# Kernel optimization log

Hardware: AMD Instinct MI355X
Metric: run time of the kernel (lower is better)

The kernel has to match this reference:

```python
import jax, jax.numpy as jnp
import numpy as np

B, S, E = 512, 200, 128
H, D = 4, 32  # att_head_nums, singlehead_emb_size; H*D == E (required by residual)
FF = 4 * H * D


def setup_inputs() -> dict:
    key = jax.random.key(0)
    ks = jax.random.split(key, 12)
    sc = 0.02
    return {
        "queries": jax.random.normal(ks[0], (B, S, E), jnp.float32),
        "keys": jax.random.normal(ks[1], (B, S, E), jnp.float32),
        "keys_mask": jax.random.randint(ks[2], (B, S), 0, 2) > 0,
        "Wq": jax.random.normal(ks[3], (H * D, E), jnp.float32) * sc,
        "bq": jnp.zeros((H * D,), jnp.float32),
        "Wk": jax.random.normal(ks[4], (H * D, E), jnp.float32) * sc,
        "bk": jnp.zeros((H * D,), jnp.float32),
        "Wv": jax.random.normal(ks[5], (H * D, E), jnp.float32) * sc,
        "bv": jnp.zeros((H * D,), jnp.float32),
        "W1": jax.random.normal(ks[6], (FF, H * D), jnp.float32) * sc,
        "b1": jnp.zeros((FF,), jnp.float32),
        "W2": jax.random.normal(ks[7], (H * D, FF), jnp.float32) * sc,
        "b2": jnp.zeros((H * D,), jnp.float32),
    }


def reference(queries, keys, keys_mask, Wq, bq, Wk, bk, Wv, bv, W1, b1, W2, b2):
    # QKV projections (nn.Linear: x @ W.T + b)
    Q = queries @ Wq.T + bq                         # [B,S,H*D]
    K = keys @ Wk.T + bk
    V = keys @ Wv.T + bv
    Qh = Q.reshape(B, S, H, D).transpose(0, 2, 1, 3)  # [B,H,S,D]
    Kh = K.reshape(B, S, H, D).transpose(0, 2, 1, 3)
    Vh = V.reshape(B, S, H, D).transpose(0, 2, 1, 3)
    scores = jnp.einsum('bhqd,bhkd->bhqk', Qh, Kh) / jnp.sqrt(jnp.float32(D))
    scores = jnp.where(keys_mask[:, None, None, :], scores, -jnp.inf)
    probs = jax.nn.softmax(scores, axis=-1)
    out = jnp.einsum('bhqk,bhkd->bhqd', probs, Vh)   # [B,H,S,D]
    out = out.transpose(0, 2, 1, 3).reshape(B, S, H * D)
    out = out + queries                              # residual (use_res=True)
    # FFN with residual (use_feed_forward=True, no layer norm, dropout=0)
    ff = jax.nn.relu(out @ W1.T + b1) @ W2.T + b2
    return ff + out
```

## Files before the change

kernel.cpp:

```cpp
#include <hip/hip_runtime.h>

#define B_  512
#define S_  200
#define M_  102400

typedef short bf16x8 __attribute__((ext_vector_type(8)));
typedef float f32x4  __attribute__((ext_vector_type(4)));
typedef unsigned short u16;
typedef u16 us4 __attribute__((ext_vector_type(4)));
typedef unsigned int u32;

#define MFMA16 __builtin_amdgcn_mfma_f32_16x16x32_bf16
#define GLDS(gp, lp) __builtin_amdgcn_global_load_lds( \
    (const __attribute__((address_space(1))) unsigned int*)(gp), \
    (__attribute__((address_space(3))) unsigned int*)(lp), 16, 0, 0)

__device__ __forceinline__ u16 f2bf(float f) {
    union { float f; unsigned u; } v; v.f = f;
    unsigned r = v.u + 0x7fffu + ((v.u >> 16) & 1u);
    return (u16)(r >> 16);
}
__device__ __forceinline__ float bf2f(u16 x) {
    union { unsigned u; float f; } v; v.u = ((unsigned)x) << 16;
    return v.f;
}
__device__ __forceinline__ u32 pk(float a, float b) {
    return (__float_as_uint(a) >> 16) | (__float_as_uint(b) & 0xffff0000u);
}
__device__ __forceinline__ int swz(int row, int b) { return b ^ ((row & 7) << 4); }

#define WQ_OFF   0
#define WK_OFF   16384
#define WV_OFF   32768
#define W1_OFF   49152
#define W2_OFF   114688
#define BQS_OFF  180224
#define QB_OFF   262144
#define KB_OFF   (QB_OFF + 13107200)
#define VB_OFF   (KB_OFF + 13107200)

__global__ __launch_bounds__(256) void cvt_kernel(
    const float* __restrict__ Wq, const float* __restrict__ bq,
    const float* __restrict__ Wk, const float* __restrict__ Wv,
    const float* __restrict__ W1, const float* __restrict__ W2,
    u16* __restrict__ wdst, float* __restrict__ bqs)
{
    const float QSC = 0.17677669529663689f * 1.4426950408889634f;
    int idx = blockIdx.x * 256 + threadIdx.x;
    if (idx < 128) bqs[idx] = bq[idx] * QSC;
    if (idx < 49152) {
        int wsel = idx >> 14, r = (idx >> 7) & 127, c = idx & 127;
        const float* src = wsel == 0 ? Wq : (wsel == 1 ? Wk : Wv);
        float v = src[idx & 16383];
        if (wsel == 0) v *= QSC;
        *(u16*)((char*)(wdst + wsel * 16384) + r * 256 + swz(r, 2 * c)) = f2bf(v);
    } else if (idx < 114688) {
        int i = idx - 49152;
        int r_g = i >> 7, c = i & 127;
        int sub = r_g >> 6, fr = r_g & 63;
        *(u16*)((char*)(wdst + W1_OFF) + sub * 16384 + fr * 256 + ((2 * c) ^ ((fr & 7) << 4)))
            = f2bf(W1[i]);
    } else if (idx < 180224) {
        int i = idx - 114688;
        int r_out = i >> 9, c_ff = i & 511;
        int sub = c_ff >> 6, o = c_ff & 63;
        int chunk = o >> 5, w32 = o & 31;
        int bb = w32 >> 4, hh = (w32 >> 2) & 3, rr = w32 & 3;
        int lc = chunk * 32 + 8 * hh + 4 * bb + rr;
        *(u16*)((char*)(wdst + W2_OFF) + sub * 16384 + r_out * 128 + ((2 * lc) ^ ((r_out & 7) << 4)))
            = f2bf(W2[i]);
    }
}

__global__ __launch_bounds__(256) void proj_q_kernel(
    const float* __restrict__ X, const u16* __restrict__ Ws,
    const float* __restrict__ bqs, u16* __restrict__ Y)
{
    __shared__ __align__(16) u16 sW[16384];
    const int tid = threadIdx.x, w = tid >> 6, lane = tid & 63;
    const int lo = lane & 15, hi = lane >> 4;
    const int base = blockIdx.x * 128;

#pragma unroll
    for (int k = 0; k < 8; ++k) {
        int seg = w * 8 + k;
        GLDS((const char*)Ws + seg * 1024 + lane * 16, (char*)sW + seg * 1024);
    }

    bf16x8 a[2][4];
#pragma unroll
    for (int t = 0; t < 2; ++t) {
        const float* rp = X + (size_t)(base + w * 32 + t * 16 + lo) * 128;
#pragma unroll
        for (int ks = 0; ks < 4; ++ks) {
            float4 v0 = *(const float4*)(rp + ks * 32 + hi * 8);
            float4 v1 = *(const float4*)(rp + ks * 32 + hi * 8 + 4);
            union { bf16x8 v; u16 s[8]; } af;
            af.s[0]=f2bf(v0.x); af.s[1]=f2bf(v0.y); af.s[2]=f2bf(v0.z); af.s[3]=f2bf(v0.w);
            af.s[4]=f2bf(v1.x); af.s[5]=f2bf(v1.y); af.s[6]=f2bf(v1.z); af.s[7]=f2bf(v1.w);
            a[t][ks] = af.v;
        }
    }
    asm volatile("s_waitcnt vmcnt(0)" ::: "memory");
    __builtin_amdgcn_s_barrier();

#pragma unroll
    for (int n = 0; n < 8; ++n) {
        bf16x8 bf[4];
#pragma unroll
        for (int ks = 0; ks < 4; ++ks)
            bf[ks] = *(const bf16x8*)((const char*)sW + (n*16+lo)*256 + swz(lo, ks*64 + hi*16));
        float bb = bqs[n * 16 + lo];
#pragma unroll
        for (int t = 0; t < 2; ++t) {
            f32x4 acc = {0.f, 0.f, 0.f, 0.f};
#pragma unroll
            for (int ks = 0; ks < 4; ++ks) acc = MFMA16(a[t][ks], bf[ks], acc, 0, 0, 0);
#pragma unroll
            for (int r = 0; r < 4; ++r) {
                int row = base + w * 32 + t * 16 + hi * 4 + r;
                *(u16*)((char*)Y + (size_t)row * 256 + swz(row, n * 32 + 2 * lo)) =
                    f2bf(acc[r] + bb);
            }
        }
    }
}

__global__ __launch_bounds__(256) void proj_kv_kernel(
    const float* __restrict__ X, const u16* __restrict__ Wks, const u16* __restrict__ Wvs,
    const float* __restrict__ bk, const float* __restrict__ bv,
    u16* __restrict__ K, u16* __restrict__ V)
{
    __shared__ __align__(16) u16 sWk[16384];
    __shared__ __align__(16) u16 sWv[16384];
    const int tid = threadIdx.x, w = tid >> 6, lane = tid & 63;
    const int lo = lane & 15, hi = lane >> 4;
    const int base = blockIdx.x * 128;

#pragma unroll
    for (int k = 0; k < 8; ++k) {
        int seg = w * 8 + k;
        GLDS((const char*)Wks + seg * 1024 + lane * 16, (char*)sWk + seg * 1024);
        GLDS((const char*)Wvs + seg * 1024 + lane * 16, (char*)sWv + seg * 1024);
    }

    bf16x8 a[2][4];
#pragma unroll
    for (int t = 0; t < 2; ++t) {
        const float* rp = X + (size_t)(base + w * 32 + t * 16 + lo) * 128;
#pragma unroll
        for (int ks = 0; ks < 4; ++ks) {
            float4 v0 = *(const float4*)(rp + ks * 32 + hi * 8);
            float4 v1 = *(const float4*)(rp + ks * 32 + hi * 8 + 4);
            union { bf16x8 v; u16 s[8]; } af;
            af.s[0]=f2bf(v0.x); af.s[1]=f2bf(v0.y); af.s[2]=f2bf(v0.z); af.s[3]=f2bf(v0.w);
            af.s[4]=f2bf(v1.x); af.s[5]=f2bf(v1.y); af.s[6]=f2bf(v1.z); af.s[7]=f2bf(v1.w);
            a[t][ks] = af.v;
        }
    }
    asm volatile("s_waitcnt vmcnt(0)" ::: "memory");
    __builtin_amdgcn_s_barrier();

#pragma unroll
    for (int n = 0; n < 8; ++n) {
        bf16x8 bf[4];
#pragma unroll
        for (int ks = 0; ks < 4; ++ks)
            bf[ks] = *(const bf16x8*)((const char*)sWk + (n*16+lo)*256 + swz(lo, ks*64 + hi*16));
        float bb = bk[n * 16 + lo];
#pragma unroll
        for (int t = 0; t < 2; ++t) {
            f32x4 acc = {0.f, 0.f, 0.f, 0.f};
#pragma unroll
            for (int ks = 0; ks < 4; ++ks) acc = MFMA16(a[t][ks], bf[ks], acc, 0, 0, 0);
#pragma unroll
            for (int r = 0; r < 4; ++r) {
                size_t row = base + w * 32 + t * 16 + hi * 4 + r;
                K[row * 128 + n * 16 + lo] = f2bf(acc[r] + bb);
            }
        }
    }
#pragma unroll
    for (int n = 0; n < 8; ++n) {
        bf16x8 bf[4];
#pragma unroll
        for (int ks = 0; ks < 4; ++ks)
            bf[ks] = *(const bf16x8*)((const char*)sWv + (n*16+lo)*256 + swz(lo, ks*64 + hi*16));
        float bb = bv[n * 16 + lo];
#pragma unroll
        for (int t = 0; t < 2; ++t) {
            f32x4 acc = {0.f, 0.f, 0.f, 0.f};
#pragma unroll
            for (int ks = 0; ks < 4; ++ks) acc = MFMA16(a[t][ks], bf[ks], acc, 0, 0, 0);
#pragma unroll
            for (int r = 0; r < 4; ++r) {
                size_t row = base + w * 32 + t * 16 + hi * 4 + r;
                V[row * 128 + n * 16 + lo] = f2bf(acc[r] + bb);
            }
        }
    }
}

__global__ __launch_bounds__(256, 4) void attn_kernel(
    const u16* __restrict__ Qb, const u16* __restrict__ Kb, const u16* __restrict__ Vb,
    const int* __restrict__ mask, const float* __restrict__ queries, u16* __restrict__ Xb)
{
    __shared__ __align__(16) u16 sK[224][40];
    __shared__ __align__(16) u16 sVt[32][248];
    __shared__ __align__(16) u16 sMk[224];
    __shared__ u16 sIdx[224];
    __shared__ int sCnt4[4];

    const int bid = blockIdx.x;
    const int wg  = (bid & 7) * 256 + (bid >> 3);
    const int b   = wg >> 2;
    const int h   = wg & 3;
    const int tid = threadIdx.x;
    const int w = tid >> 6, lane = tid & 63;
    const int lo = lane & 15, hi = lane >> 4;
    const size_t rowbase = (size_t)b * 200;

    bool valid = (tid < 200) && (mask[rowbase + tid] != 0);
    unsigned long long bal = __ballot(valid);
    int prefix = __popcll(bal & ((1ull << lane) - 1ull));
    if (lane == 0) sCnt4[w] = __popcll(bal);
    __syncthreads();

    int c0_ = sCnt4[0], c1_ = sCnt4[1], c2_ = sCnt4[2], c3_ = sCnt4[3];
    int off = (w > 0 ? c0_ : 0) + (w > 1 ? c1_ : 0) + (w > 2 ? c2_ : 0);
    const int cnt = c0_ + c1_ + c2_ + c3_;
    const int cntPad = (cnt + 31) & ~31;
    const int nch = cntPad >> 5;
    if (valid) sIdx[off + prefix] = (u16)tid;
    for (int i = tid; i < 224; i += 256) {
        int cb = i & ~31, local = i & 31;
        int hh = local >> 3, j = local & 7;
        int slot = cb + 16 * (j >> 2) + 4 * hh + (j & 3);
        sMk[i] = (slot < cnt) ? (u16)0x3F80 : (u16)0;
    }
    __syncthreads();

    for (int i = tid; i < (cntPad << 2); i += 256) {
        int j = i >> 2, part = i & 3;
        bf16x8 val = {0,0,0,0,0,0,0,0};
        if (j < cnt) {
            int key = sIdx[j];
            val = *(const bf16x8*)(Kb + (rowbase + key) * 128 + h * 32 + part * 8);
        }
        *(bf16x8*)&sK[j][part * 8] = val;
    }
    for (int slot = tid; slot < (cntPad << 3); slot += 256) {
        int d = slot & 31, sg = slot >> 5;
        int s0 = sg * 4;
        int cb = s0 & ~31, a = (s0 & 31) >> 2;
        int pos = cb + (a & 3) * 8 + (a >> 2) * 4;
        us4 v;
#pragma unroll
        for (int j = 0; j < 4; ++j) {
            int s = s0 + j;
            v[j] = (s < cnt) ? Vb[(rowbase + sIdx[s]) * 128 + h * 32 + d] : (u16)0;
        }
        *(us4*)&sVt[d][pos] = v;
    }
    __syncthreads();

    for (int qb = w; qb < 13; qb += 4) {
        int qrow = qb * 16 + lo;
        if (qrow > 199) qrow = 199;
        bf16x8 qf = *(const bf16x8*)((const char*)Qb + (size_t)(rowbase + qrow) * 256
                                      + swz(qrow, h * 64 + hi * 16));

        f32x4 acc0 = {0.f, 0.f, 0.f, 0.f};
        f32x4 acc1 = {0.f, 0.f, 0.f, 0.f};
        f32x4 accs = {0.f, 0.f, 0.f, 0.f};

#pragma unroll 1
        for (int kt = 0; kt < nch; ++kt) {
            int cb = kt * 32;
            bf16x8 k0 = *(const bf16x8*)&sK[cb + lo][hi * 8];
            bf16x8 k1 = *(const bf16x8*)&sK[cb + 16 + lo][hi * 8];
            f32x4 z = {0.f, 0.f, 0.f, 0.f};
            f32x4 s0 = MFMA16(k0, qf, z, 0, 0, 0);
            f32x4 s1 = MFMA16(k1, qf, z, 0, 0, 0);
            float p0 = __builtin_amdgcn_exp2f(s0[0]);
            float p1 = __builtin_amdgcn_exp2f(s0[1]);
            float p2 = __builtin_amdgcn_exp2f(s0[2]);
            float p3 = __builtin_amdgcn_exp2f(s0[3]);
            float p4 = __builtin_amdgcn_exp2f(s1[0]);
            float p5 = __builtin_amdgcn_exp2f(s1[1]);
            float p6 = __builtin_amdgcn_exp2f(s1[2]);
            float p7 = __builtin_amdgcn_exp2f(s1[3]);
            union { bf16x8 v; u32 d[4]; } pa;
            pa.d[0] = pk(p0, p1); pa.d[1] = pk(p2, p3);
            pa.d[2] = pk(p4, p5); pa.d[3] = pk(p6, p7);
            bf16x8 mkf = *(const bf16x8*)&sMk[cb + hi * 8];
            bf16x8 v0  = *(const bf16x8*)&sVt[lo][cb + hi * 8];
            bf16x8 v1  = *(const bf16x8*)&sVt[16 + lo][cb + hi * 8];
            acc0 = MFMA16(pa.v, v0, acc0, 0, 0, 0);
            acc1 = MFMA16(pa.v, v1, acc1, 0, 0, 0);
            accs = MFMA16(pa.v, mkf, accs, 0, 0, 0);
        }

        float invr[4];
#pragma unroll
        for (int r = 0; r < 4; ++r) invr[r] = __builtin_amdgcn_rcpf(accs[r]);
#pragma unroll
        for (int r = 0; r < 4; ++r) {
            int row = qb * 16 + hi * 4 + r;
            if (row < 200) {
                size_t o  = (rowbase + row) * 128 + h * 32;
                size_t rb = (rowbase + row) * 256;
                *(u16*)((char*)Xb + rb + swz(row, h * 64 + 2 * lo)) =
                    f2bf(acc0[r] * invr[r] + queries[o + lo]);
                *(u16*)((char*)Xb + rb + swz(row, h * 64 + 32 + 2 * lo)) =
                    f2bf(acc1[r] * invr[r] + queries[o + 16 + lo]);
            }
        }
    }
}

__global__ __launch_bounds__(256, 2) void ffn_kernel(
    const u16* __restrict__ Xb, const u16* __restrict__ W1s, const u16* __restrict__ W2s,
    const float* __restrict__ b1, const float* __restrict__ b2, float* __restrict__ out)
{
    __shared__ __align__(16) u16 sW1[2][8192];
    __shared__ __align__(16) u16 sW2[2][8192];
    const int tid = threadIdx.x, w = tid >> 6, lane = tid & 63;
    const int lo = lane & 15, hi = lane >> 4;
    const size_t base = (size_t)blockIdx.x * 128;
    const int wrow = w * 32;

#pragma unroll
    for (int k = 0; k < 4; ++k) {
        int seg = w * 4 + k;
        GLDS((const char*)W1s + seg * 1024 + lane * 16, (char*)sW1[0] + seg * 1024);
        GLDS((const char*)W2s + seg * 1024 + lane * 16, (char*)sW2[0] + seg * 1024);
    }

    bf16x8 a[2][4];
#pragma unroll
    for (int t = 0; t < 2; ++t) {
        size_t row = base + wrow + t * 16 + lo;
#pragma unroll
        for (int ks = 0; ks < 4; ++ks)
            a[t][ks] = *(const bf16x8*)((const char*)Xb + row * 256
                                         + ((ks * 64 + hi * 16) ^ ((lo & 7) << 4)));
    }

    f32x4 yacc[2][8];
#pragma unroll
    for (int t = 0; t < 2; ++t)
#pragma unroll
        for (int n = 0; n < 8; ++n) yacc[t][n] = (f32x4){0.f, 0.f, 0.f, 0.f};

    asm volatile("s_waitcnt vmcnt(0)" ::: "memory");
    __builtin_amdgcn_s_barrier();

    for (int sub = 0; sub < 8; ++sub) {
        int cur = sub & 1, nxt = cur ^ 1;
        if (sub < 7) {
#pragma unroll
            for (int k = 0; k < 4; ++k) {
                int seg = w * 4 + k;
                GLDS((const char*)W1s + (sub + 1) * 16384 + seg * 1024 + lane * 16,
                     (char*)sW1[nxt] + seg * 1024);
                GLDS((const char*)W2s + (sub + 1) * 16384 + seg * 1024 + lane * 16,
                     (char*)sW2[nxt] + seg * 1024);
            }
        }
#pragma unroll
        for (int c = 0; c < 2; ++c) {
            bf16x8 w1f[2][4];
#pragma unroll
            for (int u = 0; u < 2; ++u)
#pragma unroll
                for (int ks = 0; ks < 4; ++ks)
                    w1f[u][ks] = *(const bf16x8*)((const char*)sW1[cur]
                                   + ((2*c+u) * 16 + lo) * 256
                                   + ((ks * 64 + hi * 16) ^ ((lo & 7) << 4)));
            float4 b1v0 = *(const float4*)(b1 + sub * 64 + (2*c) * 16 + 4 * hi);
            float4 b1v1 = *(const float4*)(b1 + sub * 64 + (2*c+1) * 16 + 4 * hi);
            bf16x8 pb[2];
#pragma unroll
            for (int t = 0; t < 2; ++t) {
                f32x4 h0 = {0.f,0.f,0.f,0.f}, h1 = {0.f,0.f,0.f,0.f};
#pragma unroll
                for (int ks = 0; ks < 4; ++ks) {
                    h0 = MFMA16(w1f[0][ks], a[t][ks], h0, 0, 0, 0);
                    h1 = MFMA16(w1f[1][ks], a[t][ks], h1, 0, 0, 0);
                }
                float p0 = fmaxf(h0[0] + b1v0.x, 0.f);
                float p1 = fmaxf(h0[1] + b1v0.y, 0.f);
                float p2 = fmaxf(h0[2] + b1v0.z, 0.f);
                float p3 = fmaxf(h0[3] + b1v0.w, 0.f);
                float p4 = fmaxf(h1[0] + b1v1.x, 0.f);
                float p5 = fmaxf(h1[1] + b1v1.y, 0.f);
                float p6 = fmaxf(h1[2] + b1v1.z, 0.f);
                float p7 = fmaxf(h1[3] + b1v1.w, 0.f);
                union { bf16x8 v; u32 d[4]; } pu;
                pu.d[0] = pk(p0, p1); pu.d[1] = pk(p2, p3);
                pu.d[2] = pk(p4, p5); pu.d[3] = pk(p6, p7);
                pb[t] = pu.v;
            }
#pragma unroll
            for (int n = 0; n < 8; ++n) {
                bf16x8 w2f = *(const bf16x8*)((const char*)sW2[cur]
                               + (n * 16 + lo) * 128
                               + ((c * 64 + hi * 16) ^ ((lo & 7) << 4)));
                yacc[0][n] = MFMA16(w2f, pb[0], yacc[0][n], 0, 0, 0);
                yacc[1][n] = MFMA16(w2f, pb[1], yacc[1][n], 0, 0, 0);
            }
        }
        asm volatile("s_waitcnt vmcnt(0)" ::: "memory");
        __builtin_amdgcn_s_barrier();
    }

#pragma unroll
    for (int t = 0; t < 2; ++t) {
        size_t row = base + wrow + t * 16 + lo;
#pragma unroll
        for (int n = 0; n < 8; ++n) {
            float4 b2v = *(const float4*)(b2 + n * 16 + 4 * hi);
            us4 rv = *(const us4*)((const char*)Xb + row * 256
                                    + ((2 * (n * 16 + 4 * hi)) ^ (((int)row & 7) << 4)));
            float4 o;
            o.x = yacc[t][n][0] + b2v.x + bf2f(rv[0]);
            o.y = yacc[t][n][1] + b2v.y + bf2f(rv[1]);
            o.z = yacc[t][n][2] + b2v.z + bf2f(rv[2]);
            o.w = yacc[t][n][3] + b2v.w + bf2f(rv[3]);
            *(float4*)(out + row * 128 + n * 16 + 4 * hi) = o;
        }
    }
}

extern "C" void kernel_launch(void* const* d_in, const int* in_sizes, int n_in,
                              void* d_out, int out_size, void* d_ws, size_t ws_size,
                              hipStream_t stream) {
    const float* queries = (const float*)d_in[0];
    const float* keys    = (const float*)d_in[1];
    const int*   mask    = (const int*)d_in[2];
    const float* Wq = (const float*)d_in[3];
    const float* bq = (const float*)d_in[4];
    const float* Wk = (const float*)d_in[5];
    const float* bk = (const float*)d_in[6];
    const float* Wv = (const float*)d_in[7];
    const float* bv = (const float*)d_in[8];
    const float* W1 = (const float*)d_in[9];
    const float* b1 = (const float*)d_in[10];
    const float* W2 = (const float*)d_in[11];
    const float* b2 = (const float*)d_in[12];
    float* out = (float*)d_out;

    u16* wbase = (u16*)d_ws;
    u16* Qb = wbase + QB_OFF;
    u16* Kb = wbase + KB_OFF;
    u16* Vb = wbase + VB_OFF;
    float* bqs = (float*)(wbase + BQS_OFF);

    cvt_kernel<<<704, 256, 0, stream>>>(Wq, bq, Wk, Wv, W1, W2, wbase, bqs);
    proj_q_kernel<<<800, 256, 0, stream>>>(queries, wbase + WQ_OFF, bqs, Qb);
    proj_kv_kernel<<<800, 256, 0, stream>>>(keys, wbase + WK_OFF, wbase + WV_OFF,
                                            bk, bv, Kb, Vb);
    attn_kernel<<<B_ * 4, 256, 0, stream>>>(Qb, Kb, Vb, mask, queries, Qb);
    ffn_kernel<<<800, 256, 0, stream>>>(Qb, wbase + W1_OFF, wbase + W2_OFF, b1, b2, out);
}
```

Before: 127.9 us.

## Single-buffer FFN weight tiles and reorder GEMM phases to raise occupancy

Replaces the double-buffered W1/W2 LDS tiles with single buffers, halving shared memory per block, and raises the launch-bounds occupancy hint from 2 to 5 blocks. The loop is split so all W1 GEMMs finish before the next W1 tile is loaded, and all W2 GEMMs finish before the next W2 tile is loaded, with an extra barrier per iteration. The aim is to hide load latency through more resident waves instead of explicit prefetch. In exchange, each block gets less intra-block overlap and more synchronisation, and the tighter register budget could cause spills.

```diff
diff --git a/kernel.cpp b/kernel.cpp
--- a/kernel.cpp
+++ b/kernel.cpp
@@ -319,12 +319,12 @@
     }
 }
 
-__global__ __launch_bounds__(256, 2) void ffn_kernel(
+__global__ __launch_bounds__(256, 5) void ffn_kernel(
     const u16* __restrict__ Xb, const u16* __restrict__ W1s, const u16* __restrict__ W2s,
     const float* __restrict__ b1, const float* __restrict__ b2, float* __restrict__ out)
 {
-    __shared__ __align__(16) u16 sW1[2][8192];
-    __shared__ __align__(16) u16 sW2[2][8192];
+    __shared__ __align__(16) u16 sW1[8192];
+    __shared__ __align__(16) u16 sW2[8192];
     const int tid = threadIdx.x, w = tid >> 6, lane = tid & 63;
     const int lo = lane & 15, hi = lane >> 4;
     const size_t base = (size_t)blockIdx.x * 128;
@@ -333,8 +333,8 @@
 #pragma unroll
     for (int k = 0; k < 4; ++k) {
         int seg = w * 4 + k;
-        GLDS((const char*)W1s + seg * 1024 + lane * 16, (char*)sW1[0] + seg * 1024);
-        GLDS((const char*)W2s + seg * 1024 + lane * 16, (char*)sW2[0] + seg * 1024);
+        GLDS((const char*)W1s + seg * 1024 + lane * 16, (char*)sW1 + seg * 1024);
+        GLDS((const char*)W2s + seg * 1024 + lane * 16, (char*)sW2 + seg * 1024);
     }
 
     bf16x8 a[2][4];
@@ -357,17 +357,7 @@
     __builtin_amdgcn_s_barrier();
 
     for (int sub = 0; sub < 8; ++sub) {
-        int cur = sub & 1, nxt = cur ^ 1;
-        if (sub < 7) {
-#pragma unroll
-            for (int k = 0; k < 4; ++k) {
-                int seg = w * 4 + k;
-                GLDS((const char*)W1s + (sub + 1) * 16384 + seg * 1024 + lane * 16,
-                     (char*)sW1[nxt] + seg * 1024);
-                GLDS((const char*)W2s + (sub + 1) * 16384 + seg * 1024 + lane * 16,
-                     (char*)sW2[nxt] + seg * 1024);
-            }
-        }
+        bf16x8 pbAll[2][2];
 #pragma unroll
         for (int c = 0; c < 2; ++c) {
             bf16x8 w1f[2][4];
@@ -375,12 +365,11 @@
             for (int u = 0; u < 2; ++u)
 #pragma unroll
                 for (int ks = 0; ks < 4; ++ks)
-                    w1f[u][ks] = *(const bf16x8*)((const char*)sW1[cur]
+                    w1f[u][ks] = *(const bf16x8*)((const char*)sW1
                                    + ((2*c+u) * 16 + lo) * 256
                                    + ((ks * 64 + hi * 16) ^ ((lo & 7) << 4)));
             float4 b1v0 = *(const float4*)(b1 + sub * 64 + (2*c) * 16 + 4 * hi);
             float4 b1v1 = *(const float4*)(b1 + sub * 64 + (2*c+1) * 16 + 4 * hi);
-            bf16x8 pb[2];
 #pragma unroll
             for (int t = 0; t < 2; ++t) {
                 f32x4 h0 = {0.f,0.f,0.f,0.f}, h1 = {0.f,0.f,0.f,0.f};
@@ -400,19 +389,40 @@
                 union { bf16x8 v; u32 d[4]; } pu;
                 pu.d[0] = pk(p0, p1); pu.d[1] = pk(p2, p3);
                 pu.d[2] = pk(p4, p5); pu.d[3] = pk(p6, p7);
-                pb[t] = pu.v;
-            }
+                pbAll[c][t] = pu.v;
+            }
+        }
+        asm volatile("s_waitcnt vmcnt(0)" ::: "memory");
+        __builtin_amdgcn_s_barrier();
+        if (sub < 7) {
+#pragma unroll
+            for (int k = 0; k < 4; ++k) {
+                int seg = w * 4 + k;
+                GLDS((const char*)W1s + (sub + 1) * 16384 + seg * 1024 + lane * 16,
+                     (char*)sW1 + seg * 1024);
+            }
+        }
+#pragma unroll
+        for (int c = 0; c < 2; ++c) {
 #pragma unroll
             for (int n = 0; n < 8; ++n) {
-                bf16x8 w2f = *(const bf16x8*)((const char*)sW2[cur]
+                bf16x8 w2f = *(const bf16x8*)((const char*)sW2
                                + (n * 16 + lo) * 128
                                + ((c * 64 + hi * 16) ^ ((lo & 7) << 4)));
-                yacc[0][n] = MFMA16(w2f, pb[0], yacc[0][n], 0, 0, 0);
-                yacc[1][n] = MFMA16(w2f, pb[1], yacc[1][n], 0, 0, 0);
+                yacc[0][n] = MFMA16(w2f, pbAll[c][0], yacc[0][n], 0, 0, 0);
+                yacc[1][n] = MFMA16(w2f, pbAll[c][1], yacc[1][n], 0, 0, 0);
             }
         }
         asm volatile("s_waitcnt vmcnt(0)" ::: "memory");
         __builtin_amdgcn_s_barrier();
+        if (sub < 7) {
+#pragma unroll
+            for (int k = 0; k < 4; ++k) {
+                int seg = w * 4 + k;
+                GLDS((const char*)W2s + (sub + 1) * 16384 + seg * 1024 + lane * 16,
+                     (char*)sW2 + seg * 1024);
+            }
+        }
     }
 
 #pragma unroll
```

Measured after the change: 378.5 us. +196.0%, slower.

## Software-pipeline FFN so second GEMM of chunk s-1 overlaps first GEMM of chunk s

Applied to the files above, without the earlier changes.

Restructures the FFN kernel loop so the W2 GEMM for the previous hidden chunk runs at the start of the next iteration, alongside the W1 GEMM for the current chunk. W2 tiles are now loaded one step later, into the buffer matching the current iteration, and the relu'd activations are carried across iterations in registers, with an epilogue that drains the last chunk. The goal is to break the dependency from the W1 MFMA through bias+relu+pack into the W2 MFMA and expose more independent MFMA work. In exchange it uses more registers for the carried activations, which may affect occupancy.

```diff
diff --git a/kernel.cpp b/kernel.cpp
--- a/kernel.cpp
+++ b/kernel.cpp
@@ -334,7 +334,6 @@
     for (int k = 0; k < 4; ++k) {
         int seg = w * 4 + k;
         GLDS((const char*)W1s + seg * 1024 + lane * 16, (char*)sW1[0] + seg * 1024);
-        GLDS((const char*)W2s + seg * 1024 + lane * 16, (char*)sW2[0] + seg * 1024);
     }
 
     bf16x8 a[2][4];
@@ -356,16 +355,36 @@
     asm volatile("s_waitcnt vmcnt(0)" ::: "memory");
     __builtin_amdgcn_s_barrier();
 
-    for (int sub = 0; sub < 8; ++sub) {
-        int cur = sub & 1, nxt = cur ^ 1;
-        if (sub < 7) {
+    bf16x8 pbPrev[2][2];
+
+#pragma unroll 2
+    for (int s = 0; s < 8; ++s) {
+        const int cur = s & 1, nxt = cur ^ 1;
+        if (s < 7) {
 #pragma unroll
             for (int k = 0; k < 4; ++k) {
                 int seg = w * 4 + k;
-                GLDS((const char*)W1s + (sub + 1) * 16384 + seg * 1024 + lane * 16,
+                GLDS((const char*)W1s + (s + 1) * 16384 + seg * 1024 + lane * 16,
                      (char*)sW1[nxt] + seg * 1024);
-                GLDS((const char*)W2s + (sub + 1) * 16384 + seg * 1024 + lane * 16,
-                     (char*)sW2[nxt] + seg * 1024);
+            }
+        }
+#pragma unroll
+        for (int k = 0; k < 4; ++k) {
+            int seg = w * 4 + k;
+            GLDS((const char*)W2s + s * 16384 + seg * 1024 + lane * 16,
+                 (char*)sW2[cur] + seg * 1024);
+        }
+        if (s > 0) {
+#pragma unroll
+            for (int c = 0; c < 2; ++c) {
+#pragma unroll
+                for (int n = 0; n < 8; ++n) {
+                    bf16x8 w2f = *(const bf16x8*)((const char*)sW2[nxt]
+                                   + (n * 16 + lo) * 128
+                                   + ((c * 64 + hi * 16) ^ ((lo & 7) << 4)));
+                    yacc[0][n] = MFMA16(w2f, pbPrev[c][0], yacc[0][n], 0, 0, 0);
+                    yacc[1][n] = MFMA16(w2f, pbPrev[c][1], yacc[1][n], 0, 0, 0);
+                }
             }
         }
 #pragma unroll
@@ -378,9 +397,8 @@
                     w1f[u][ks] = *(const bf16x8*)((const char*)sW1[cur]
                                    + ((2*c+u) * 16 + lo) * 256
                                    + ((ks * 64 + hi * 16) ^ ((lo & 7) << 4)));
-            float4 b1v0 = *(const float4*)(b1 + sub * 64 + (2*c) * 16 + 4 * hi);
-            float4 b1v1 = *(const float4*)(b1 + sub * 64 + (2*c+1) * 16 + 4 * hi);
-            bf16x8 pb[2];
+            float4 b1v0 = *(const float4*)(b1 + s * 64 + (2*c) * 16 + 4 * hi);
+            float4 b1v1 = *(const float4*)(b1 + s * 64 + (2*c+1) * 16 + 4 * hi);
 #pragma unroll
             for (int t = 0; t < 2; ++t) {
                 f32x4 h0 = {0.f,0.f,0.f,0.f}, h1 = {0.f,0.f,0.f,0.f};
@@ -400,19 +418,23 @@
                 union { bf16x8 v; u32 d[4]; } pu;
                 pu.d[0] = pk(p0, p1); pu.d[1] = pk(p2, p3);
                 pu.d[2] = pk(p4, p5); pu.d[3] = pk(p6, p7);
-                pb[t] = pu.v;
-            }
-#pragma unroll
-            for (int n = 0; n < 8; ++n) {
-                bf16x8 w2f = *(const bf16x8*)((const char*)sW2[cur]
-                               + (n * 16 + lo) * 128
-                               + ((c * 64 + hi * 16) ^ ((lo & 7) << 4)));
-                yacc[0][n] = MFMA16(w2f, pb[0], yacc[0][n], 0, 0, 0);
-                yacc[1][n] = MFMA16(w2f, pb[1], yacc[1][n], 0, 0, 0);
+                pbPrev[c][t] = pu.v;
             }
         }
         asm volatile("s_waitcnt vmcnt(0)" ::: "memory");
         __builtin_amdgcn_s_barrier();
+    }
+
+#pragma unroll
+    for (int c = 0; c < 2; ++c) {
+#pragma unroll
+        for (int n = 0; n < 8; ++n) {
+            bf16x8 w2f = *(const bf16x8*)((const char*)sW2[1]
+                           + (n * 16 + lo) * 128
+                           + ((c * 64 + hi * 16) ^ ((lo & 7) << 4)));
+            yacc[0][n] = MFMA16(w2f, pbPrev[c][0], yacc[0][n], 0, 0, 0);
+            yacc[1][n] = MFMA16(w2f, pbPrev[c][1], yacc[1][n], 0, 0, 0);
+        }
     }
 
 #pragma unroll
```

Result: no change. 127.2 us (-0.5%).

## Software-pipeline FFN with 32-wide subtiles, triple-buffered weights, skewed GEMM2

Applied to the files above, without the earlier changes.

The FFN kernel now processes the hidden dimension in sixteen 32-wide slices instead of eight 64-wide ones. W1 and W2 tiles are triple-buffered in LDS, and the second GEMM for slice s-1 is interleaved with the first GEMM for slice s. Partial vmcnt waits replace full drains, and b1 is staged in LDS. The weight pre-swizzle layout is changed to match. The aim is to hide global-to-LDS latency and MFMA dependency stalls, at the cost of more iterations and barriers and a delicate vmcnt accounting.

```diff
diff --git a/kernel.cpp b/kernel.cpp
--- a/kernel.cpp
+++ b/kernel.cpp
@@ -57,18 +57,17 @@
     } else if (idx < 114688) {
         int i = idx - 49152;
         int r_g = i >> 7, c = i & 127;
-        int sub = r_g >> 6, fr = r_g & 63;
-        *(u16*)((char*)(wdst + W1_OFF) + sub * 16384 + fr * 256 + ((2 * c) ^ ((fr & 7) << 4)))
+        int sub = r_g >> 5, fr = r_g & 31;
+        *(u16*)((char*)(wdst + W1_OFF) + sub * 8192 + fr * 256 + ((2 * c) ^ ((fr & 7) << 4)))
             = f2bf(W1[i]);
     } else if (idx < 180224) {
         int i = idx - 114688;
         int r_out = i >> 9, c_ff = i & 511;
-        int sub = c_ff >> 6, o = c_ff & 63;
-        int chunk = o >> 5, w32 = o & 31;
+        int s32 = c_ff >> 5, w32 = c_ff & 31;
         int bb = w32 >> 4, hh = (w32 >> 2) & 3, rr = w32 & 3;
-        int lc = chunk * 32 + 8 * hh + 4 * bb + rr;
-        *(u16*)((char*)(wdst + W2_OFF) + sub * 16384 + r_out * 128 + ((2 * lc) ^ ((r_out & 7) << 4)))
-            = f2bf(W2[i]);
+        int lc = 8 * hh + 4 * bb + rr;
+        *(u16*)((char*)(wdst + W2_OFF) + s32 * 8192 + r_out * 64
+                + ((2 * lc) ^ (((r_out >> 1) & 3) << 4))) = f2bf(W2[i]);
     }
 }
 
@@ -323,19 +322,15 @@
     const u16* __restrict__ Xb, const u16* __restrict__ W1s, const u16* __restrict__ W2s,
     const float* __restrict__ b1, const float* __restrict__ b2, float* __restrict__ out)
 {
-    __shared__ __align__(16) u16 sW1[2][8192];
-    __shared__ __align__(16) u16 sW2[2][8192];
+    __shared__ __align__(16) u16 sW1[3][4096];
+    __shared__ __align__(16) u16 sW2[3][4096];
+    __shared__ __align__(16) float sB1[512];
     const int tid = threadIdx.x, w = tid >> 6, lane = tid & 63;
     const int lo = lane & 15, hi = lane >> 4;
     const size_t base = (size_t)blockIdx.x * 128;
     const int wrow = w * 32;
 
-#pragma unroll
-    for (int k = 0; k < 4; ++k) {
-        int seg = w * 4 + k;
-        GLDS((const char*)W1s + seg * 1024 + lane * 16, (char*)sW1[0] + seg * 1024);
-        GLDS((const char*)W2s + seg * 1024 + lane * 16, (char*)sW2[0] + seg * 1024);
-    }
+    float bv0 = b1[tid], bv1 = b1[tid + 256];
 
     bf16x8 a[2][4];
 #pragma unroll
@@ -346,6 +341,14 @@
             a[t][ks] = *(const bf16x8*)((const char*)Xb + row * 256
                                          + ((ks * 64 + hi * 16) ^ ((lo & 7) << 4)));
     }
+#pragma unroll
+    for (int k = 0; k < 2; ++k) {
+        int seg = w * 2 + k;
+        GLDS((const char*)W1s + seg * 1024 + lane * 16, (char*)sW1[0] + seg * 1024);
+        GLDS((const char*)W1s + 8192 + seg * 1024 + lane * 16, (char*)sW1[1] + seg * 1024);
+        GLDS((const char*)W2s + seg * 1024 + lane * 16, (char*)sW2[0] + seg * 1024);
+    }
+    sB1[tid] = bv0; sB1[tid + 256] = bv1;
 
     f32x4 yacc[2][8];
 #pragma unroll
@@ -353,34 +356,50 @@
 #pragma unroll
         for (int n = 0; n < 8; ++n) yacc[t][n] = (f32x4){0.f, 0.f, 0.f, 0.f};
 
-    asm volatile("s_waitcnt vmcnt(0)" ::: "memory");
-    __builtin_amdgcn_s_barrier();
-
-    for (int sub = 0; sub < 8; ++sub) {
-        int cur = sub & 1, nxt = cur ^ 1;
-        if (sub < 7) {
-#pragma unroll
-            for (int k = 0; k < 4; ++k) {
-                int seg = w * 4 + k;
-                GLDS((const char*)W1s + (sub + 1) * 16384 + seg * 1024 + lane * 16,
-                     (char*)sW1[nxt] + seg * 1024);
-                GLDS((const char*)W2s + (sub + 1) * 16384 + seg * 1024 + lane * 16,
-                     (char*)sW2[nxt] + seg * 1024);
-            }
-        }
-#pragma unroll
-        for (int c = 0; c < 2; ++c) {
+    __syncthreads();
+
+    bf16x8 pbPrev[2];
+
+#pragma unroll
+    for (int s = 0; s < 16; ++s) {
+        const int bw1 = s % 3, bw2p = (s + 2) % 3;
+        if (s + 2 < 16) {
+#pragma unroll
+            for (int k = 0; k < 2; ++k) {
+                int seg = w * 2 + k;
+                GLDS((const char*)W1s + (s + 2) * 8192 + seg * 1024 + lane * 16,
+                     (char*)sW1[(s + 2) % 3] + seg * 1024);
+            }
+        }
+        if (s + 1 < 16) {
+#pragma unroll
+            for (int k = 0; k < 2; ++k) {
+                int seg = w * 2 + k;
+                GLDS((const char*)W2s + (s + 1) * 8192 + seg * 1024 + lane * 16,
+                     (char*)sW2[(s + 1) % 3] + seg * 1024);
+            }
+        }
+        if (s > 0) {
+#pragma unroll
+            for (int n = 0; n < 8; ++n) {
+                bf16x8 w2f = *(const bf16x8*)((const char*)sW2[bw2p]
+                               + (n * 16 + lo) * 64
+                               + ((hi * 16) ^ (((lo >> 1) & 3) << 4)));
+                yacc[0][n] = MFMA16(w2f, pbPrev[0], yacc[0][n], 0, 0, 0);
+                yacc[1][n] = MFMA16(w2f, pbPrev[1], yacc[1][n], 0, 0, 0);
+            }
+        }
+        {
             bf16x8 w1f[2][4];
 #pragma unroll
             for (int u = 0; u < 2; ++u)
 #pragma unroll
                 for (int ks = 0; ks < 4; ++ks)
-                    w1f[u][ks] = *(const bf16x8*)((const char*)sW1[cur]
-                                   + ((2*c+u) * 16 + lo) * 256
+                    w1f[u][ks] = *(const bf16x8*)((const char*)sW1[bw1]
+                                   + (u * 16 + lo) * 256
                                    + ((ks * 64 + hi * 16) ^ ((lo & 7) << 4)));
-            float4 b1v0 = *(const float4*)(b1 + sub * 64 + (2*c) * 16 + 4 * hi);
-            float4 b1v1 = *(const float4*)(b1 + sub * 64 + (2*c+1) * 16 + 4 * hi);
-            bf16x8 pb[2];
+            float4 b1v0 = *(const float4*)&sB1[s * 32 + 4 * hi];
+            float4 b1v1 = *(const float4*)&sB1[s * 32 + 16 + 4 * hi];
 #pragma unroll
             for (int t = 0; t < 2; ++t) {
                 f32x4 h0 = {0.f,0.f,0.f,0.f}, h1 = {0.f,0.f,0.f,0.f};
@@ -400,19 +419,26 @@
                 union { bf16x8 v; u32 d[4]; } pu;
                 pu.d[0] = pk(p0, p1); pu.d[1] = pk(p2, p3);
                 pu.d[2] = pk(p4, p5); pu.d[3] = pk(p6, p7);
-                pb[t] = pu.v;
-            }
-#pragma unroll
-            for (int n = 0; n < 8; ++n) {
-                bf16x8 w2f = *(const bf16x8*)((const char*)sW2[cur]
-                               + (n * 16 + lo) * 128
-                               + ((c * 64 + hi * 16) ^ ((lo & 7) << 4)));
-                yacc[0][n] = MFMA16(w2f, pb[0], yacc[0][n], 0, 0, 0);
-                yacc[1][n] = MFMA16(w2f, pb[1], yacc[1][n], 0, 0, 0);
-            }
-        }
-        asm volatile("s_waitcnt vmcnt(0)" ::: "memory");
+                pbPrev[t] = pu.v;
+            }
+        }
+        if (s <= 13) {
+            asm volatile("s_waitcnt vmcnt(4)" ::: "memory");
+        } else if (s == 14) {
+            asm volatile("s_waitcnt vmcnt(2)" ::: "memory");
+        } else {
+            asm volatile("s_waitcnt vmcnt(0)" ::: "memory");
+        }
         __builtin_amdgcn_s_barrier();
+    }
+
+#pragma unroll
+    for (int n = 0; n < 8; ++n) {
+        bf16x8 w2f = *(const bf16x8*)((const char*)sW2[0]
+                       + (n * 16 + lo) * 64
+                       + ((hi * 16) ^ (((lo >> 1) & 3) << 4)));
+        yacc[0][n] = MFMA16(w2f, pbPrev[0], yacc[0][n], 0, 0, 0);
+        yacc[1][n] = MFMA16(w2f, pbPrev[1], yacc[1][n], 0, 0, 0);
     }
 
 #pragma unroll
```

New measurement: 129.5 us. No clear change (+1.2%).
